# Performance work log

Measured on AMD Instinct MI355X. Metric: run time of the kernel, lower is better.

Reference implementation:

```python
import jax, jax.numpy as jnp
import numpy as np

B = 1_048_576
NUM_ITERS = 10  # training-mode default; eval mode uses 1000
EPS = 1e-12
LOW, HIGH = 0.02, 0.98  # SquashedSigmoid bounds


def setup_inputs() -> dict:
    key = jax.random.key(0)
    ks = jax.random.split(key, 4)
    # margins are population masses -> keep strictly positive
    margins = jax.random.uniform(ks[0], (B, 8), dtype=jnp.float32) + 0.1

    def lin(k, i, o):
        return (jax.random.normal(k, (i, o), jnp.float32) / np.sqrt(i)).astype(jnp.float32)

    return {
        "margins": margins,
        "W1": lin(ks[1], 8, 32), "b1": jnp.zeros((32,), jnp.float32),
        "W2": lin(ks[2], 32, 16), "b2": jnp.zeros((16,), jnp.float32),
        "W3": lin(ks[3], 16, 9), "b3": jnp.zeros((9,), jnp.float32),
    }


def tau_batched(p):
    # p: (B,4) positive params -> (B,3,3) positive couples matrix.
    # 2x2 core, extended by geometric-mean row/col (user-supplied tau in repo).
    a = p.reshape(-1, 2, 2)
    col3 = jnp.sqrt(a[:, :, 0] * a[:, :, 1])          # (B,2)
    row3 = jnp.sqrt(a[:, 0, :] * a[:, 1, :])          # (B,2)
    corner = jnp.sqrt(row3[:, 0] * row3[:, 1])        # (B,)
    top = jnp.concatenate([a, col3[:, :, None]], axis=2)                 # (B,2,3)
    bot = jnp.concatenate([row3, corner[:, None]], axis=1)[:, None, :]   # (B,1,3)
    return jnp.concatenate([top, bot], axis=1)        # (B,3,3)


def sinkhorn_knopp(A, row_margins, col_margins, iters):
    # Batched Sinkhorn-Knopp: A (B,R,C), row_margins (B,R), col_margins (B,C)
    r = row_margins[:, :, None]
    c = col_margins[:, None, :]

    def body(A, _):
        A = A * (r / (A.sum(axis=2, keepdims=True) + EPS))
        A = A * (c / (A.sum(axis=1, keepdims=True) + EPS))
        return A, None

    A, _ = jax.lax.scan(body, A, None, length=iters)
    return A


def reference(margins, W1, b1, W2, b2, W3, b3):
    Bn = margins.shape[0]
    M, F = margins[:, 0:3], margins[:, 3:6]

    # MLP: Linear-ReLU-Linear-ReLU-Linear
    h = jax.nn.relu(margins @ W1 + b1)
    h = jax.nn.relu(h @ W2 + b2)
    pars = h @ W3 + b3                                   # (B,9)

    muc = tau_batched(jnp.exp(pars[:, 0:4]))             # (B,3,3)
    sqs = lambda x: LOW + (HIGH - LOW) * jax.nn.sigmoid(x)
    shm, shf = sqs(pars[:, 4:6]), sqs(pars[:, 6:8])      # (B,2) each
    V = jnp.exp(pars[:, -1])                             # (B,)

    ones = jnp.ones((Bn, 1), margins.dtype)
    shm0 = jnp.concatenate([shm, ones], axis=1)          # (B,3)
    shf0 = jnp.concatenate([shf, ones], axis=1)          # (B,3)
    mucm0, muc0f = M * shm0, F * shf0                    # matched masses (margins)
    mum0, mu0f = M * (1.0 - shm0), F * (1.0 - shf0)      # singles

    muc = sinkhorn_knopp(muc, mucm0, muc0f, NUM_ITERS)   # (B,3,3)

    top = jnp.concatenate([muc, mum0[:, :, None]], axis=2)   # (B,3,4)
    bot = jnp.concatenate(
        [mu0f[:, None, :], jnp.zeros((Bn, 1, 1), margins.dtype)], axis=2)  # (B,1,4)
    mus = jnp.concatenate([top, bot], axis=1)            # (B,4,4)
    return mus, V
```

## Files before the change

kernel.cpp:

```cpp
#include <hip/hip_runtime.h>
#include <math.h>


#define EPS_F 1e-12f
#define QLOW  0.02f
#define QSPAN 0.96f

constexpr int R = 2;

__device__ __forceinline__ float frcp(float x) { return __builtin_amdgcn_rcpf(x); }
__device__ __forceinline__ float fsig(float x) { return frcp(1.0f + __expf(-x)); }

__global__ __launch_bounds__(256) void sinkhorn_fused(
    const float* __restrict__ margins,
    const float* __restrict__ W1, const float* __restrict__ b1,
    const float* __restrict__ W2, const float* __restrict__ b2,
    const float* __restrict__ W3, const float* __restrict__ b3,
    float* __restrict__ out, int n)
{
    __shared__ __align__(16) float sW1[256];
    __shared__ __align__(16) float sW2[512];
    __shared__ __align__(16) float sW3T[144];
    __shared__ __align__(16) float sB1[32];
    __shared__ __align__(16) float sB2[16];
    __shared__ __align__(16) float sB3[12];

    {
        const int t = threadIdx.x;
        sW1[t] = W1[t];
        sW2[t] = W2[t];
        sW2[t + 256] = W2[t + 256];
        if (t < 144) { const int k = t / 9, j = t - 9 * k; sW3T[j * 16 + k] = W3[t]; }
        if (t < 32) sB1[t] = b1[t];
        if (t < 16) sB2[t] = b2[t];
        if (t < 9)  sB3[t] = b3[t];
    }
    __syncthreads();

    const float4* __restrict__ sW1v  = (const float4*)sW1;
    const float4* __restrict__ sW2v  = (const float4*)sW2;
    const float4* __restrict__ sW3Tv = (const float4*)sW3T;

    const int tid  = blockIdx.x * blockDim.x + threadIdx.x;
    const int lane = tid & 63;
    const int base = (tid >> 6) * (64 * R) + lane;

    const float4* __restrict__ m4 = (const float4*)margins;

    float m[R][8];
#pragma unroll
    for (int r = 0; r < R; ++r) {
        const int row = base + 64 * r;
        const float4 a0 = m4[row * 2 + 0];
        const float4 a1 = m4[row * 2 + 1];
        m[r][0] = a0.x; m[r][1] = a0.y; m[r][2] = a0.z; m[r][3] = a0.w;
        m[r][4] = a1.x; m[r][5] = a1.y; m[r][6] = a1.z; m[r][7] = a1.w;
    }

    float h1[R][32];
#pragma unroll
    for (int j = 0; j < 32; ++j) {
        const float bb = sB1[j];
#pragma unroll
        for (int r = 0; r < R; ++r) h1[r][j] = bb;
    }
#pragma unroll
    for (int k = 0; k < 8; ++k) {
#pragma unroll
        for (int j4 = 0; j4 < 8; ++j4) {
            const float4 w = sW1v[k * 8 + j4];
#pragma unroll
            for (int r = 0; r < R; ++r) {
                h1[r][j4*4+0] = fmaf(m[r][k], w.x, h1[r][j4*4+0]);
                h1[r][j4*4+1] = fmaf(m[r][k], w.y, h1[r][j4*4+1]);
                h1[r][j4*4+2] = fmaf(m[r][k], w.z, h1[r][j4*4+2]);
                h1[r][j4*4+3] = fmaf(m[r][k], w.w, h1[r][j4*4+3]);
            }
        }
    }
#pragma unroll
    for (int j = 0; j < 32; ++j)
#pragma unroll
        for (int r = 0; r < R; ++r) h1[r][j] = fmaxf(h1[r][j], 0.0f);

    float h2[R][16];
#pragma unroll
    for (int j = 0; j < 16; ++j) {
        const float bb = sB2[j];
#pragma unroll
        for (int r = 0; r < R; ++r) h2[r][j] = bb;
    }
#pragma unroll
    for (int k = 0; k < 32; ++k) {
#pragma unroll
        for (int j4 = 0; j4 < 4; ++j4) {
            const float4 w = sW2v[k * 4 + j4];
#pragma unroll
            for (int r = 0; r < R; ++r) {
                h2[r][j4*4+0] = fmaf(h1[r][k], w.x, h2[r][j4*4+0]);
                h2[r][j4*4+1] = fmaf(h1[r][k], w.y, h2[r][j4*4+1]);
                h2[r][j4*4+2] = fmaf(h1[r][k], w.z, h2[r][j4*4+2]);
                h2[r][j4*4+3] = fmaf(h1[r][k], w.w, h2[r][j4*4+3]);
            }
        }
    }
#pragma unroll
    for (int j = 0; j < 16; ++j)
#pragma unroll
        for (int r = 0; r < R; ++r) h2[r][j] = fmaxf(h2[r][j], 0.0f);

    float p[R][9];
#pragma unroll
    for (int j = 0; j < 9; ++j) {
#pragma unroll
        for (int r = 0; r < R; ++r) p[r][j] = sB3[j];
#pragma unroll
        for (int k4 = 0; k4 < 4; ++k4) {
            const float4 w = sW3Tv[j * 4 + k4];
#pragma unroll
            for (int r = 0; r < R; ++r) {
                p[r][j] = fmaf(h2[r][k4*4+0], w.x, p[r][j]);
                p[r][j] = fmaf(h2[r][k4*4+1], w.y, p[r][j]);
                p[r][j] = fmaf(h2[r][k4*4+2], w.z, p[r][j]);
                p[r][j] = fmaf(h2[r][k4*4+3], w.w, p[r][j]);
            }
        }
    }

    float4* __restrict__ o4 = (float4*)out;
    float* __restrict__ oV = out + (size_t)n * 16;

#pragma unroll
    for (int r = 0; r < R; ++r) {
        const int row = base + 64 * r;

        const float e0 = __expf(p[r][0]);
        const float e1 = __expf(p[r][1]);
        const float e2 = __expf(p[r][2]);
        const float e3 = __expf(p[r][3]);
        const float col0 = sqrtf(e0 * e1);
        const float col1 = sqrtf(e2 * e3);
        const float rw0  = sqrtf(e0 * e2);
        const float rw1  = sqrtf(e1 * e3);
        const float corn = sqrtf(rw0 * rw1);

        const float a00 = e0,  a01 = e1,  a02 = col0;
        const float a10 = e2,  a11 = e3,  a12 = col1;
        const float a20 = rw0, a21 = rw1, a22 = corn;

        const float s4 = QLOW + QSPAN * fsig(p[r][4]);
        const float s5 = QLOW + QSPAN * fsig(p[r][5]);
        const float s6 = QLOW + QSPAN * fsig(p[r][6]);
        const float s7 = QLOW + QSPAN * fsig(p[r][7]);

        const float M0 = m[r][0], M1 = m[r][1], M2 = m[r][2];
        const float F0 = m[r][3], F1 = m[r][4], F2 = m[r][5];

        const float rm0 = M0 * s4, rm1 = M1 * s5, rm2 = M2;
        const float cm0 = F0 * s6, cm1 = F1 * s7, cm2 = F2;
        const float um0 = M0 * (1.0f - s4);
        const float um1 = M1 * (1.0f - s5);
        const float uf0 = F0 * (1.0f - s6);
        const float uf1 = F1 * (1.0f - s7);

        float u0 = 1.0f, u1 = 1.0f, u2 = 1.0f;
        float v0 = 1.0f, v1 = 1.0f, v2 = 1.0f;
#pragma unroll
        for (int it = 0; it < 10; ++it) {
            float t0 = fmaf(a02, v2, fmaf(a01, v1, a00 * v0));
            float t1 = fmaf(a12, v2, fmaf(a11, v1, a10 * v0));
            float t2 = fmaf(a22, v2, fmaf(a21, v1, a20 * v0));
            u0 = u0 * rm0 * frcp(fmaf(u0, t0, EPS_F));
            u1 = u1 * rm1 * frcp(fmaf(u1, t1, EPS_F));
            u2 = u2 * rm2 * frcp(fmaf(u2, t2, EPS_F));
            float s0 = fmaf(a20, u2, fmaf(a10, u1, a00 * u0));
            float s1 = fmaf(a21, u2, fmaf(a11, u1, a01 * u0));
            float s2 = fmaf(a22, u2, fmaf(a12, u1, a02 * u0));
            v0 = v0 * cm0 * frcp(fmaf(v0, s0, EPS_F));
            v1 = v1 * cm1 * frcp(fmaf(v1, s1, EPS_F));
            v2 = v2 * cm2 * frcp(fmaf(v2, s2, EPS_F));
        }

        const float A0f = u0 * a00 * v0, A1f = u0 * a01 * v1, A2f = u0 * a02 * v2;
        const float A3f = u1 * a10 * v0, A4f = u1 * a11 * v1, A5f = u1 * a12 * v2;
        const float A6f = u2 * a20 * v0, A7f = u2 * a21 * v1, A8f = u2 * a22 * v2;

        o4[row * 4 + 0] = make_float4(A0f, A1f, A2f, um0);
        o4[row * 4 + 1] = make_float4(A3f, A4f, A5f, um1);
        o4[row * 4 + 2] = make_float4(A6f, A7f, A8f, 0.0f);
        o4[row * 4 + 3] = make_float4(uf0, uf1, 0.0f, 0.0f);
        oV[row] = __expf(p[r][8]);
    }
}

extern "C" void kernel_launch(void* const* d_in, const int* in_sizes, int n_in,
                              void* d_out, int out_size, void* d_ws, size_t ws_size,
                              hipStream_t stream) {
    const float* margins = (const float*)d_in[0];
    const float* W1 = (const float*)d_in[1];
    const float* b1 = (const float*)d_in[2];
    const float* W2 = (const float*)d_in[3];
    const float* b2 = (const float*)d_in[4];
    const float* W3 = (const float*)d_in[5];
    const float* b3 = (const float*)d_in[6];

    const int n = in_sizes[0] / 8;
    const int threads = n / R;
    dim3 block(256), grid(threads / 256);

    sinkhorn_fused<<<grid, block, 0, stream>>>(margins, W1, b1, W2, b2, W3, b3,
                                               (float*)d_out, n);
}
```

Measured before the change: 132.4 us.

## Fuse first MLP layer into second via transposed W1 and double rows per thread

W1 is now stored transposed in shared memory, so each hidden unit of layer 1 is computed as a dot product and consumed immediately by layer 2. This removes the 32-wide h1 register array. The freed registers allow four rows per thread instead of two, which amortizes the shared-memory weight loads over more rows. The trade-off is a smaller grid and possibly higher register pressure or lower occupancy for a kernel that is largely memory-bound.

After: 145.7 us. 1.1x slower.

```diff
diff --git a/kernel.cpp b/kernel.cpp
--- a/kernel.cpp
+++ b/kernel.cpp
@@ -6,7 +6,7 @@
 #define QLOW  0.02f
 #define QSPAN 0.96f
 
-constexpr int R = 2;
+constexpr int R = 4;
 
 __device__ __forceinline__ float frcp(float x) { return __builtin_amdgcn_rcpf(x); }
 __device__ __forceinline__ float fsig(float x) { return frcp(1.0f + __expf(-x)); }
@@ -18,7 +18,7 @@
     const float* __restrict__ W3, const float* __restrict__ b3,
     float* __restrict__ out, int n)
 {
-    __shared__ __align__(16) float sW1[256];
+    __shared__ __align__(16) float sW1T[256];
     __shared__ __align__(16) float sW2[512];
     __shared__ __align__(16) float sW3T[144];
     __shared__ __align__(16) float sB1[32];
@@ -27,7 +27,7 @@
 
     {
         const int t = threadIdx.x;
-        sW1[t] = W1[t];
+        { const int j = t >> 3, k = t & 7; sW1T[t] = W1[k * 32 + j]; }
         sW2[t] = W2[t];
         sW2[t + 256] = W2[t + 256];
         if (t < 144) { const int k = t / 9, j = t - 9 * k; sW3T[j * 16 + k] = W3[t]; }
@@ -37,7 +37,7 @@
     }
     __syncthreads();
 
-    const float4* __restrict__ sW1v  = (const float4*)sW1;
+    const float4* __restrict__ sW1Tv = (const float4*)sW1T;
     const float4* __restrict__ sW2v  = (const float4*)sW2;
     const float4* __restrict__ sW3Tv = (const float4*)sW3T;
 
@@ -57,32 +57,6 @@
         m[r][4] = a1.x; m[r][5] = a1.y; m[r][6] = a1.z; m[r][7] = a1.w;
     }
 
-    float h1[R][32];
-#pragma unroll
-    for (int j = 0; j < 32; ++j) {
-        const float bb = sB1[j];
-#pragma unroll
-        for (int r = 0; r < R; ++r) h1[r][j] = bb;
-    }
-#pragma unroll
-    for (int k = 0; k < 8; ++k) {
-#pragma unroll
-        for (int j4 = 0; j4 < 8; ++j4) {
-            const float4 w = sW1v[k * 8 + j4];
-#pragma unroll
-            for (int r = 0; r < R; ++r) {
-                h1[r][j4*4+0] = fmaf(m[r][k], w.x, h1[r][j4*4+0]);
-                h1[r][j4*4+1] = fmaf(m[r][k], w.y, h1[r][j4*4+1]);
-                h1[r][j4*4+2] = fmaf(m[r][k], w.z, h1[r][j4*4+2]);
-                h1[r][j4*4+3] = fmaf(m[r][k], w.w, h1[r][j4*4+3]);
-            }
-        }
-    }
-#pragma unroll
-    for (int j = 0; j < 32; ++j)
-#pragma unroll
-        for (int r = 0; r < R; ++r) h1[r][j] = fmaxf(h1[r][j], 0.0f);
-
     float h2[R][16];
 #pragma unroll
     for (int j = 0; j < 16; ++j) {
@@ -90,17 +64,35 @@
 #pragma unroll
         for (int r = 0; r < R; ++r) h2[r][j] = bb;
     }
-#pragma unroll
-    for (int k = 0; k < 32; ++k) {
+
+#pragma unroll
+    for (int j = 0; j < 32; ++j) {
+        const float4 wa = sW1Tv[j * 2 + 0];
+        const float4 wb = sW1Tv[j * 2 + 1];
+        const float bj = sB1[j];
+        float h[R];
+#pragma unroll
+        for (int r = 0; r < R; ++r) {
+            float x = bj;
+            x = fmaf(m[r][0], wa.x, x);
+            x = fmaf(m[r][1], wa.y, x);
+            x = fmaf(m[r][2], wa.z, x);
+            x = fmaf(m[r][3], wa.w, x);
+            x = fmaf(m[r][4], wb.x, x);
+            x = fmaf(m[r][5], wb.y, x);
+            x = fmaf(m[r][6], wb.z, x);
+            x = fmaf(m[r][7], wb.w, x);
+            h[r] = fmaxf(x, 0.0f);
+        }
 #pragma unroll
         for (int j4 = 0; j4 < 4; ++j4) {
-            const float4 w = sW2v[k * 4 + j4];
+            const float4 w = sW2v[j * 4 + j4];
 #pragma unroll
             for (int r = 0; r < R; ++r) {
-                h2[r][j4*4+0] = fmaf(h1[r][k], w.x, h2[r][j4*4+0]);
-                h2[r][j4*4+1] = fmaf(h1[r][k], w.y, h2[r][j4*4+1]);
-                h2[r][j4*4+2] = fmaf(h1[r][k], w.z, h2[r][j4*4+2]);
-                h2[r][j4*4+3] = fmaf(h1[r][k], w.w, h2[r][j4*4+3]);
+                h2[r][j4*4+0] = fmaf(h[r], w.x, h2[r][j4*4+0]);
+                h2[r][j4*4+1] = fmaf(h[r], w.y, h2[r][j4*4+1]);
+                h2[r][j4*4+2] = fmaf(h[r], w.z, h2[r][j4*4+2]);
+                h2[r][j4*4+3] = fmaf(h[r], w.w, h2[r][j4*4+3]);
             }
         }
     }
@@ -112,8 +104,9 @@
     float p[R][9];
 #pragma unroll
     for (int j = 0; j < 9; ++j) {
-#pragma unroll
-        for (int r = 0; r < R; ++r) p[r][j] = sB3[j];
+        const float bb = sB3[j];
+#pragma unroll
+        for (int r = 0; r < R; ++r) p[r][j] = bb;
 #pragma unroll
         for (int k4 = 0; k4 < 4; ++k4) {
             const float4 w = sW3Tv[j * 4 + k4];
```
